# Kernel tuning notes

Hardware: AMD Instinct MI355X
Metric: run time of the kernel (lower is better)

The kernel has to match this reference:

```python
import jax, jax.numpy as jnp
import numpy as np
from jax import lax

N_SAMPLES1 = 128   # self.n_samples[0]
K = 64             # k in sample_and_group
RADIUS = 0.4       # self.radius[0]
BN_EPS = 1e-5
NEG_INF = -1e8
DIMS0 = [6, 64, 64, 128]      # mlps_in[0][0] -> mlps[0]
DIMS1 = [131, 128, 128, 512]  # 128+3 -> mlps[1] (use_light_weight=False)


def _fps(pos, n):
    # pos: (N,3) -> (n,) indices; deterministic start at point 0
    Np = pos.shape[0]
    def body(carry, _):
        dists, last = carry
        d = jnp.sum((pos - pos[last]) ** 2, axis=-1)
        dists = jnp.minimum(dists, d)
        return (dists, jnp.argmax(dists).astype(jnp.int32)), last
    _, idxs = lax.scan(body, (jnp.full((Np,), 1e10, pos.dtype), jnp.int32(0)), None, length=n)
    return idxs


def _gather(values, idx):
    # values (B,N,C), idx (B,...) -> (B,...,C)
    return jax.vmap(lambda v, i: v[i])(values, idx)


def _conv_bn_relu(x, W, b, g, be):
    # 1x1 Conv2d + BatchNorm2d (training-mode batch stats) + ReLU; x (B,n,k,Cin)
    y = jnp.einsum('bnkc,cd->bnkd', x, W) + b
    m = jnp.mean(y, axis=(0, 1, 2), keepdims=True)
    v = jnp.mean(jnp.square(y - m), axis=(0, 1, 2), keepdims=True)
    return jax.nn.relu((y - m) * lax.rsqrt(v + BN_EPS) * g + be)


def _forward(x, pos,
             W00, b00, g00, be00, W01, b01, g01, be01, W02, b02, g02, be02,
             W10, b10, g10, be10, W11, b11, g11, be11, W12, b12, g12, be12):
    # ---- stage 0: FPS + kNN grouping + conv-MLP + radius-masked max pool ----
    fidx = jax.vmap(lambda p: _fps(p, N_SAMPLES1))(pos)          # (B,128)
    sp = _gather(pos, fidx)                                      # (B,128,3) sampled_pos
    # squared pairwise distances (||a||^2+||b||^2-2ab); topk/mask on sq dist is
    # equivalent to topk/mask on sqrt dist (monotone), avoids sqrt(0) NaN grads
    sq = (jnp.sum(sp ** 2, -1)[:, :, None] + jnp.sum(pos ** 2, -1)[:, None, :]
          - 2.0 * jnp.einsum('bmd,bnd->bmn', sp, pos))           # (B,128,N)
    sq = jnp.maximum(sq, 0.0)
    neg, tidx = lax.top_k(-sq, K)                                # smallest-k
    topk_sq = -neg                                               # (B,128,64)
    gp = _gather(pos, tidx) - sp[:, :, None, :]                  # centered grouped pos
    gf = jnp.concatenate([gp, _gather(x, tidx)], axis=-1)        # (B,128,64,6)
    for (W, b, g, be) in ((W00, b00, g00, be00), (W01, b01, g01, be01), (W02, b02, g02, be02)):
        gf = _conv_bn_relu(gf, W, b, g, be)                      # (B,128,64,128)
    mask = topk_sq <= RADIUS * RADIUS
    x1 = jnp.max(jnp.where(mask[..., None], gf, NEG_INF), axis=2)  # (B,128,128)
    # ---- stage 1: global (n_samples == 1) ----
    g2 = jnp.concatenate([sp, x1], axis=-1)[:, None]             # (B,1,128,131)
    for (W, b, g, be) in ((W10, b10, g10, be10), (W11, b11, g11, be11), (W12, b12, g12, be12)):
        g2 = _conv_bn_relu(g2, W, b, g, be)                      # (B,1,128,512)
    global_x = jnp.max(g2[:, 0], axis=1, keepdims=True)          # (B,1,512)
    return global_x


def setup_inputs() -> dict:
    key = jax.random.key(0)
    ks = jax.random.split(key, 16)
    B, N = 16, 8192
    inp = {
        'x': jax.random.normal(ks[0], (B, N, 3), jnp.float32),
        'pos': jax.random.uniform(ks[1], (B, N, 3), jnp.float32),
    }
    ki = 2
    for li, dims in enumerate([DIMS0, DIMS1]):
        for ci in range(3):
            cin, cout = dims[ci], dims[ci + 1]
            inp[f'W{li}{ci}'] = jax.random.normal(ks[ki], (cin, cout), jnp.float32) * 0.05
            inp[f'b{li}{ci}'] = jnp.zeros((cout,), jnp.float32)
            inp[f'g{li}{ci}'] = jnp.ones((cout,), jnp.float32)
            inp[f'be{li}{ci}'] = jnp.zeros((cout,), jnp.float32)
            ki += 1
    return inp


def reference(x, pos,
              W00, b00, g00, be00, W01, b01, g01, be01, W02, b02, g02, be02,
              W10, b10, g10, be10, W11, b11, g11, be11, W12, b12, g12, be12):
    global_x = _forward(x, pos,
                        W00, b00, g00, be00, W01, b01, g01, be01, W02, b02, g02, be02,
                        W10, b10, g10, be10, W11, b11, g11, be11, W12, b12, g12, be12)
    pos_out = jnp.zeros((pos.shape[0], 1, 3), pos.dtype)
    return global_x, pos_out
```

## Files before the change

kernel.cpp:

```cpp
#include <hip/hip_runtime.h>
#include <cstdint>
#include <cstddef>

#define NPTS 8192
#define BATCH 16
#define MS 128
#define KNB 64
#define NBLK (BATCH * MS)

__device__ __forceinline__ float dpp_wave_max_f32(float v) {
  v = fmaxf(v, __int_as_float(__builtin_amdgcn_update_dpp((int)0xff800000, __float_as_int(v), 0x111, 0xf, 0xf, false)));
  v = fmaxf(v, __int_as_float(__builtin_amdgcn_update_dpp((int)0xff800000, __float_as_int(v), 0x112, 0xf, 0xf, false)));
  v = fmaxf(v, __int_as_float(__builtin_amdgcn_update_dpp((int)0xff800000, __float_as_int(v), 0x114, 0xf, 0xf, false)));
  v = fmaxf(v, __int_as_float(__builtin_amdgcn_update_dpp((int)0xff800000, __float_as_int(v), 0x118, 0xf, 0xf, false)));
  v = fmaxf(v, __int_as_float(__builtin_amdgcn_update_dpp((int)0xff800000, __float_as_int(v), 0x142, 0xa, 0xf, false)));
  v = fmaxf(v, __int_as_float(__builtin_amdgcn_update_dpp((int)0xff800000, __float_as_int(v), 0x143, 0xc, 0xf, false)));
  return v;
}

__device__ __forceinline__ float dpp_wave_min_f32(float v) {
  v = fminf(v, __int_as_float(__builtin_amdgcn_update_dpp(0x7f800000, __float_as_int(v), 0x111, 0xf, 0xf, false)));
  v = fminf(v, __int_as_float(__builtin_amdgcn_update_dpp(0x7f800000, __float_as_int(v), 0x112, 0xf, 0xf, false)));
  v = fminf(v, __int_as_float(__builtin_amdgcn_update_dpp(0x7f800000, __float_as_int(v), 0x114, 0xf, 0xf, false)));
  v = fminf(v, __int_as_float(__builtin_amdgcn_update_dpp(0x7f800000, __float_as_int(v), 0x118, 0xf, 0xf, false)));
  v = fminf(v, __int_as_float(__builtin_amdgcn_update_dpp(0x7f800000, __float_as_int(v), 0x142, 0xa, 0xf, false)));
  v = fminf(v, __int_as_float(__builtin_amdgcn_update_dpp(0x7f800000, __float_as_int(v), 0x143, 0xc, 0xf, false)));
  return v;
}

__device__ __forceinline__ unsigned dpp_wave_min_u32(unsigned v) {
  unsigned o;
  o = (unsigned)__builtin_amdgcn_update_dpp((int)0xffffffffu, (int)v, 0x111, 0xf, 0xf, false); v = (o < v) ? o : v;
  o = (unsigned)__builtin_amdgcn_update_dpp((int)0xffffffffu, (int)v, 0x112, 0xf, 0xf, false); v = (o < v) ? o : v;
  o = (unsigned)__builtin_amdgcn_update_dpp((int)0xffffffffu, (int)v, 0x114, 0xf, 0xf, false); v = (o < v) ? o : v;
  o = (unsigned)__builtin_amdgcn_update_dpp((int)0xffffffffu, (int)v, 0x118, 0xf, 0xf, false); v = (o < v) ? o : v;
  o = (unsigned)__builtin_amdgcn_update_dpp((int)0xffffffffu, (int)v, 0x142, 0xa, 0xf, false); v = (o < v) ? o : v;
  o = (unsigned)__builtin_amdgcn_update_dpp((int)0xffffffffu, (int)v, 0x143, 0xc, 0xf, false); v = (o < v) ? o : v;
  return v;
}

__device__ __forceinline__ float dpp_row_max_f32(float v) {
  v = fmaxf(v, __int_as_float(__builtin_amdgcn_update_dpp((int)0xff800000, __float_as_int(v), 0x111, 0xf, 0xf, false)));
  v = fmaxf(v, __int_as_float(__builtin_amdgcn_update_dpp((int)0xff800000, __float_as_int(v), 0x112, 0xf, 0xf, false)));
  v = fmaxf(v, __int_as_float(__builtin_amdgcn_update_dpp((int)0xff800000, __float_as_int(v), 0x114, 0xf, 0xf, false)));
  v = fmaxf(v, __int_as_float(__builtin_amdgcn_update_dpp((int)0xff800000, __float_as_int(v), 0x118, 0xf, 0xf, false)));
  return v;
}

__device__ __forceinline__ unsigned dpp_row_min_u32(unsigned v) {
  unsigned o;
  o = (unsigned)__builtin_amdgcn_update_dpp((int)0xffffffffu, (int)v, 0x111, 0xf, 0xf, false); v = (o < v) ? o : v;
  o = (unsigned)__builtin_amdgcn_update_dpp((int)0xffffffffu, (int)v, 0x112, 0xf, 0xf, false); v = (o < v) ? o : v;
  o = (unsigned)__builtin_amdgcn_update_dpp((int)0xffffffffu, (int)v, 0x114, 0xf, 0xf, false); v = (o < v) ? o : v;
  o = (unsigned)__builtin_amdgcn_update_dpp((int)0xffffffffu, (int)v, 0x118, 0xf, 0xf, false); v = (o < v) ? o : v;
  return v;
}

#define FPS_STEP(J)                                                        \
  {                                                                        \
    const float4 p = pts4[J * 1024 + t];                                   \
    const float dx = p.x - lx;                                             \
    const float dy = p.y - ly;                                             \
    const float dz = p.z - lz;                                             \
    const float d = dx * dx + dy * dy + dz * dz;                           \
    md##J = fminf(md##J, d);                                               \
  }

#define FPS_RESCAN(J)                                                      \
  if (md##J == wv) best = (unsigned)(J * 1024 + t);

__global__ __launch_bounds__(1024, 4) void fps_kernel(const float* __restrict__ pos,
                                                      float* __restrict__ sp,
                                                      float* __restrict__ mdst,
                                                      float* __restrict__ lastst,
                                                      int it0) {
#pragma clang fp contract(off)
  extern __shared__ float4 pts4[];
  __shared__ float wval[2][16];
  __shared__ unsigned widx[2][16];
  const int b = blockIdx.x;
  const float* P = pos + (size_t)b * NPTS * 3;
  const int t = threadIdx.x;
  const int wave = t >> 6;
  const int lane = t & 63;
  float md0, md1, md2, md3, md4, md5, md6, md7;
  for (int i = t; i < NPTS; i += 1024)
    pts4[i] = make_float4(P[i * 3 + 0], P[i * 3 + 1], P[i * 3 + 2], 0.f);
  float lx, ly, lz;
  float* M = mdst + ((size_t)b * 1024 + t) * 8;
  if (it0 == 0) {
    md0 = md1 = md2 = md3 = md4 = md5 = md6 = md7 = 1e10f;
    lx = P[0]; ly = P[1]; lz = P[2];
  } else {
    const float4 a = *reinterpret_cast<const float4*>(M);
    const float4 c = *reinterpret_cast<const float4*>(M + 4);
    md0 = a.x; md1 = a.y; md2 = a.z; md3 = a.w;
    md4 = c.x; md5 = c.y; md6 = c.z; md7 = c.w;
    lx = lastst[b * 4 + 0]; ly = lastst[b * 4 + 1]; lz = lastst[b * 4 + 2];
  }
  __syncthreads();
  for (int it = it0; it < it0 + MS / 2; ++it) {
    if (t == 0) {
      sp[((size_t)b * MS + it) * 3 + 0] = lx;
      sp[((size_t)b * MS + it) * 3 + 1] = ly;
      sp[((size_t)b * MS + it) * 3 + 2] = lz;
    }
    FPS_STEP(0) FPS_STEP(1) FPS_STEP(2) FPS_STEP(3)
    FPS_STEP(4) FPS_STEP(5) FPS_STEP(6) FPS_STEP(7)
    const float m01 = fmaxf(md0, md1), m23 = fmaxf(md2, md3);
    const float m45 = fmaxf(md4, md5), m67 = fmaxf(md6, md7);
    const float bv = fmaxf(fmaxf(m01, m23), fmaxf(m45, m67));
    const float wv = __int_as_float(
        __builtin_amdgcn_readlane(__float_as_int(dpp_wave_max_f32(bv)), 63));
    unsigned best = 0xffffffffu;
    if (bv == wv) {
      FPS_RESCAN(7) FPS_RESCAN(6) FPS_RESCAN(5) FPS_RESCAN(4)
      FPS_RESCAN(3) FPS_RESCAN(2) FPS_RESCAN(1) FPS_RESCAN(0)
    }
    const unsigned wi =
        (unsigned)__builtin_amdgcn_readlane((int)dpp_wave_min_u32(best), 63);
    const int par = it & 1;
    if (lane == 0) { wval[par][wave] = wv; widx[par][wave] = wi; }
    __syncthreads();
    const float a = wval[par][lane & 15];
    const float Mx = __int_as_float(
        __builtin_amdgcn_readlane(__float_as_int(dpp_row_max_f32(a)), 15));
    const unsigned c2 = (a == Mx) ? widx[par][lane & 15] : 0xffffffffu;
    const unsigned idx =
        (unsigned)__builtin_amdgcn_readlane((int)dpp_row_min_u32(c2), 15);
    const float4 c = pts4[idx];
    lx = c.x; ly = c.y; lz = c.z;
  }
  {
    float4 a, c;
    a.x = md0; a.y = md1; a.z = md2; a.w = md3;
    c.x = md4; c.y = md5; c.z = md6; c.w = md7;
    *reinterpret_cast<float4*>(M) = a;
    *reinterpret_cast<float4*>(M + 4) = c;
    if (t == 0) {
      lastst[b * 4 + 0] = lx;
      lastst[b * 4 + 1] = ly;
      lastst[b * 4 + 2] = lz;
    }
  }
}

__global__ __launch_bounds__(256) void knn_kernel(const float* __restrict__ pos,
                                                  const float* __restrict__ xf,
                                                  const float* __restrict__ sp,
                                                  float* __restrict__ gf0,
                                                  float* __restrict__ sqsel) {
#pragma clang fp contract(off)
  __shared__ float sqv[NPTS + 32];
  __shared__ unsigned long long wlist[4][KNB];
  __shared__ unsigned long long selk[KNB];
  const int bm = blockIdx.x;
  const int b = bm >> 7;
  const float* P = pos + (size_t)b * NPTS * 3;
  const float sx = sp[bm * 3 + 0], sy = sp[bm * 3 + 1], sz = sp[bm * 3 + 2];
  const float nsp = sx * sx + sy * sy + sz * sz;
  const int t = threadIdx.x;
  const int wave = t >> 6;
  const int lane = t & 63;
  float cv;
  unsigned ci;
  {
    unsigned long long k0 = ~0ULL;
    for (int j = 0; j < 32; ++j) {
      const int i = j * 256 + t;
      const float qx = P[i * 3 + 0], qy = P[i * 3 + 1], qz = P[i * 3 + 2];
      const float npos = qx * qx + qy * qy + qz * qz;
      const float dt = sx * qx + sy * qy + sz * qz;
      float sq = (nsp + npos) - 2.0f * dt;
      sq = fmaxf(sq, 0.0f);
      sqv[i + j] = sq;
      const unsigned long long key =
          ((unsigned long long)__float_as_uint(sq) << 32) | (unsigned)i;
      if (key < k0) k0 = key;
    }
    cv = __uint_as_float((unsigned)(k0 >> 32));
    ci = (unsigned)k0;
  }
  __syncthreads();
  unsigned cmask = 0u;
  for (int round = 0; round < KNB; ++round) {
    const float wv = __int_as_float(
        __builtin_amdgcn_readlane(__float_as_int(dpp_wave_min_f32(cv)), 63));
    const unsigned sel = (cv == wv) ? ci : 0xffffffffu;
    const unsigned wi =
        (unsigned)__builtin_amdgcn_readlane((int)dpp_wave_min_u32(sel), 63);
    if (lane == 0)
      wlist[wave][round] =
          ((unsigned long long)__float_as_uint(wv) << 32) | wi;
    const int col = (int)(wi & 255u);
    const int ownerLane = col & 63;
    const unsigned jsel = wi >> 8;
    if (lane == ownerLane) cmask |= (1u << jsel);
    const unsigned omask =
        (unsigned)__builtin_amdgcn_readlane((int)cmask, ownerLane);
    float v = __uint_as_float(0x7f800000u);
    unsigned ii = 0xffffffffu;
    if (lane < 32 && !((omask >> lane) & 1u)) {
      const int i = lane * 256 + col;
      v = sqv[i + lane];
      ii = (unsigned)i;
    }
    const float mv = __int_as_float(
        __builtin_amdgcn_readlane(__float_as_int(dpp_wave_min_f32(v)), 63));
    const unsigned s2 = (v == mv) ? ii : 0xffffffffu;
    const unsigned mi =
        (unsigned)__builtin_amdgcn_readlane((int)dpp_wave_min_u32(s2), 63);
    if (lane == ownerLane) { cv = mv; ci = mi; }
  }
  __syncthreads();
  {
    const int w = wave, r = lane;
    const unsigned long long e = wlist[w][r];
    int rank = r;
#pragma unroll
    for (int w2 = 0; w2 < 4; ++w2) {
      if (w2 == w) continue;
      int lo = 0;
#pragma unroll
      for (int step = 32; step > 0; step >>= 1)
        if (lo + step <= KNB && wlist[w2][lo + step - 1] < e) lo += step;
      rank += lo;
    }
    if (rank < KNB) selk[rank] = e;
  }
  __syncthreads();
  if (t < KNB) {
    const unsigned long long e = selk[t];
    const int i = (int)(e & 0xffffffffu);
    const float* X = xf + (size_t)b * NPTS * 3;
    const size_t base = ((size_t)bm * KNB + t) * 6;
    gf0[base + 0] = P[i * 3 + 0] - sx;
    gf0[base + 1] = P[i * 3 + 1] - sy;
    gf0[base + 2] = P[i * 3 + 2] - sz;
    gf0[base + 3] = X[i * 3 + 0];
    gf0[base + 4] = X[i * 3 + 1];
    gf0[base + 5] = X[i * 3 + 2];
    sqsel[(size_t)bm * KNB + t] = __uint_as_float((unsigned)(e >> 32));
  }
}

__global__ __launch_bounds__(256) void l1_kernel(
    const float* __restrict__ gf0, const float* __restrict__ W0,
    const float* __restrict__ B0,
    float* __restrict__ psum, float* __restrict__ psq,
    float* __restrict__ y1pre) {
  __shared__ float in6[64 * 8];
  __shared__ float wbuf[384];
  __shared__ float out[64 * 65];
  const int blk = blockIdx.x;
  const int t = threadIdx.x;
  const float* G = gf0 + (size_t)blk * 384;
  for (int i = t; i < 384; i += 256) in6[(i / 6) * 8 + (i % 6)] = G[i];
  for (int i = t; i < 384; i += 256) wbuf[i] = W0[i];
  __syncthreads();
  const int r = t >> 2;
  const int c0 = (t & 3) * 16;
  float acc[16];
#pragma unroll
  for (int j = 0; j < 16; ++j) acc[j] = B0[c0 + j];
  for (int cin = 0; cin < 6; ++cin) {
    const float a = in6[r * 8 + cin];
#pragma unroll
    for (int j = 0; j < 16; ++j) acc[j] = fmaf(a, wbuf[cin * 64 + c0 + j], acc[j]);
  }
#pragma unroll
  for (int j = 0; j < 16; ++j) out[r * 65 + c0 + j] = acc[j];
  __syncthreads();
  if (t < 64) {
    float s = 0.f, q = 0.f;
    for (int r2 = 0; r2 < 64; ++r2) { const float v = out[r2 * 65 + t]; s += v; q += v * v; }
    psum[(size_t)t * NBLK + blk] = s;
    psq[(size_t)t * NBLK + blk] = q;
  }
  float* Y = y1pre + (size_t)blk * 4096;
  for (int i = t; i < 4096; i += 256) Y[i] = out[(i >> 6) * 65 + (i & 63)];
}

__global__ __launch_bounds__(256) void l2_kernel(
    const float* __restrict__ ypre, const float* __restrict__ sc,
    const float* __restrict__ sh, const float* __restrict__ W1,
    const float* __restrict__ B1,
    float* __restrict__ psum, float* __restrict__ psq,
    float* __restrict__ yout) {
  __shared__ float As[64 * 68];
  __shared__ float Bs[64 * 64];
  __shared__ float out[64 * 68];
  const int blk = blockIdx.x;
  const int t = threadIdx.x;
  const float* Y = ypre + (size_t)blk * 4096;
  for (int i = t; i < 4096; i += 256) {
    const int c = i & 63;
    As[(i >> 6) * 68 + c] = fmaxf(fmaf(Y[i], sc[c], sh[c]), 0.f);
  }
  for (int i = t; i < 4096; i += 256) Bs[i] = W1[i];
  __syncthreads();
  const int tr = t >> 4;
  const int tc4 = (t & 15) * 4;
  float acc[4][4];
#pragma unroll
  for (int s = 0; s < 4; ++s)
#pragma unroll
    for (int j = 0; j < 4; ++j) acc[s][j] = B1[tc4 + j];
  for (int k0 = 0; k0 < 64; k0 += 4) {
    float4 av[4];
#pragma unroll
    for (int s = 0; s < 4; ++s)
      av[s] = *reinterpret_cast<const float4*>(&As[(tr + 16 * s) * 68 + k0]);
#pragma unroll
    for (int kk = 0; kk < 4; ++kk) {
      const float4 bv = *reinterpret_cast<const float4*>(&Bs[(k0 + kk) * 64 + tc4]);
#pragma unroll
      for (int s = 0; s < 4; ++s) {
        const float a = (kk == 0) ? av[s].x : (kk == 1) ? av[s].y
                       : (kk == 2) ? av[s].z : av[s].w;
        acc[s][0] = fmaf(a, bv.x, acc[s][0]);
        acc[s][1] = fmaf(a, bv.y, acc[s][1]);
        acc[s][2] = fmaf(a, bv.z, acc[s][2]);
        acc[s][3] = fmaf(a, bv.w, acc[s][3]);
      }
    }
  }
#pragma unroll
  for (int s = 0; s < 4; ++s) {
    float4 o;
    o.x = acc[s][0]; o.y = acc[s][1]; o.z = acc[s][2]; o.w = acc[s][3];
    *reinterpret_cast<float4*>(&out[(tr + 16 * s) * 68 + tc4]) = o;
  }
  __syncthreads();
  if (t < 64) {
    float s = 0.f, q = 0.f;
    for (int r2 = 0; r2 < 64; ++r2) { const float v = out[r2 * 68 + t]; s += v; q += v * v; }
    psum[(size_t)t * NBLK + blk] = s;
    psq[(size_t)t * NBLK + blk] = q;
  }
  float* O = yout + (size_t)blk * 4096;
  for (int i = t; i < 4096; i += 256) O[i] = out[(i >> 6) * 68 + (i & 63)];
}

__global__ __launch_bounds__(256) void l3_kernel(
    const float* __restrict__ ypre, const float* __restrict__ sc,
    const float* __restrict__ sh, const float* __restrict__ W2,
    const float* __restrict__ B2,
    float* __restrict__ psum, float* __restrict__ psq,
    float* __restrict__ yout) {
  __shared__ float As[64 * 68];
  __shared__ float Bs[64 * 64];
  __shared__ float out[64 * 68];
  const int blk = blockIdx.x;
  const int t = threadIdx.x;
  const float* Y = ypre + (size_t)blk * 4096;
  for (int i = t; i < 4096; i += 256) {
    const int c = i & 63;
    As[(i >> 6) * 68 + c] = fmaxf(fmaf(Y[i], sc[c], sh[c]), 0.f);
  }
  const int tr = t >> 4;
  const int tc4 = (t & 15) * 4;
  for (int hc = 0; hc < 2; ++hc) {
    __syncthreads();
    for (int i = t; i < 4096; i += 256)
      Bs[i] = W2[(i >> 6) * 128 + hc * 64 + (i & 63)];
    __syncthreads();
    float acc[4][4];
#pragma unroll
    for (int s = 0; s < 4; ++s)
#pragma unroll
      for (int j = 0; j < 4; ++j) acc[s][j] = B2[hc * 64 + tc4 + j];
    for (int k0 = 0; k0 < 64; k0 += 4) {
      float4 av[4];
#pragma unroll
      for (int s = 0; s < 4; ++s)
        av[s] = *reinterpret_cast<const float4*>(&As[(tr + 16 * s) * 68 + k0]);
#pragma unroll
      for (int kk = 0; kk < 4; ++kk) {
        const float4 bv = *reinterpret_cast<const float4*>(&Bs[(k0 + kk) * 64 + tc4]);
#pragma unroll
        for (int s = 0; s < 4; ++s) {
          const float a = (kk == 0) ? av[s].x : (kk == 1) ? av[s].y
                         : (kk == 2) ? av[s].z : av[s].w;
          acc[s][0] = fmaf(a, bv.x, acc[s][0]);
          acc[s][1] = fmaf(a, bv.y, acc[s][1]);
          acc[s][2] = fmaf(a, bv.z, acc[s][2]);
          acc[s][3] = fmaf(a, bv.w, acc[s][3]);
        }
      }
    }
#pragma unroll
    for (int s = 0; s < 4; ++s) {
      float4 o;
      o.x = acc[s][0]; o.y = acc[s][1]; o.z = acc[s][2]; o.w = acc[s][3];
      *reinterpret_cast<float4*>(&out[(tr + 16 * s) * 68 + tc4]) = o;
    }
    __syncthreads();
    if (t < 64) {
      float s = 0.f, q = 0.f;
      for (int r2 = 0; r2 < 64; ++r2) { const float v = out[r2 * 68 + t]; s += v; q += v * v; }
      psum[(size_t)(hc * 64 + t) * NBLK + blk] = s;
      psq[(size_t)(hc * 64 + t) * NBLK + blk] = q;
    }
    float* O = yout + (size_t)blk * 8192;
    for (int i = t; i < 4096; i += 256)
      O[(i >> 6) * 128 + hc * 64 + (i & 63)] = out[(i >> 6) * 68 + (i & 63)];
  }
}

__global__ __launch_bounds__(128) void l4s1_kernel(
    const float* __restrict__ y3pre, const float* __restrict__ sc3,
    const float* __restrict__ sh3, const float* __restrict__ sqsel,
    const float* __restrict__ sp, const float* __restrict__ W,
    const float* __restrict__ bia, float* __restrict__ y1) {
  __shared__ float sqs[64];
  __shared__ float row[132];
  const int blk = blockIdx.x;
  const int t = threadIdx.x;
  if (t < 64) sqs[t] = sqsel[(size_t)blk * 64 + t];
  __syncthreads();
  const float scv = sc3[t], shv = sh3[t];
  const float* Y = y3pre + (size_t)blk * 8192;
  float mx = -1e8f;
  for (int r = 0; r < 64; ++r) {
    const float act = fmaxf(fmaf(Y[r * 128 + t], scv, shv), 0.f);
    const float v = (sqs[r] <= 0.16f) ? act : -1e8f;
    mx = fmaxf(mx, v);
  }
  if (t < 3) row[t] = sp[(size_t)blk * 3 + t];
  row[3 + t] = mx;
  __syncthreads();
  float acc = bia[t];
  for (int cin = 0; cin < 131; ++cin) acc = fmaf(row[cin], W[(size_t)cin * 128 + t], acc);
  y1[(size_t)blk * 128 + t] = acc;
}

__global__ __launch_bounds__(256) void p_stats(const float* __restrict__ psum,
                                               const float* __restrict__ psq,
                                               float invN,
                                               const float* __restrict__ g,
                                               const float* __restrict__ be,
                                               float* __restrict__ sc,
                                               float* __restrict__ sh) {
  const int c = blockIdx.x;
  const int t = threadIdx.x;
  double s = 0.0, q = 0.0;
  for (int k = t; k < NBLK; k += 256) {
    s += (double)psum[(size_t)c * NBLK + k];
    q += (double)psq[(size_t)c * NBLK + k];
  }
  __shared__ double ss[256], qq[256];
  ss[t] = s;
  qq[t] = q;
  __syncthreads();
  for (int st = 128; st > 0; st >>= 1) {
    if (t < st) { ss[t] += ss[t + st]; qq[t] += qq[t + st]; }
    __syncthreads();
  }
  if (t == 0) {
    const double mean = ss[0] * (double)invN;
    double var = qq[0] * (double)invN - mean * mean;
    if (var < 0.0) var = 0.0;
    const float scl = (float)((double)g[c] / sqrt(var + 1e-5));
    sc[c] = scl;
    sh[c] = be[c] - (float)mean * scl;
  }
}

__global__ __launch_bounds__(128) void s2_kernel(const float* __restrict__ y1,
                                                 const float* __restrict__ sc, const float* __restrict__ sh,
                                                 const float* __restrict__ W, const float* __restrict__ bia,
                                                 float* __restrict__ y2) {
  __shared__ float row[128];
  const int rowid = blockIdx.x;
  const int t = threadIdx.x;
  row[t] = fmaxf(fmaf(y1[(size_t)rowid * 128 + t], sc[t], sh[t]), 0.f);
  __syncthreads();
  float acc = bia[t];
  for (int cin = 0; cin < 128; ++cin) acc = fmaf(row[cin], W[(size_t)cin * 128 + t], acc);
  y2[(size_t)rowid * 128 + t] = acc;
}

__global__ __launch_bounds__(256) void s3_kernel(const float* __restrict__ y2,
                                                 const float* __restrict__ sc, const float* __restrict__ sh,
                                                 const float* __restrict__ W, const float* __restrict__ bia,
                                                 float* __restrict__ y3) {
  __shared__ float row[128];
  const int rowid = blockIdx.x;
  const int t = threadIdx.x;
  if (t < 128) row[t] = fmaxf(fmaf(y2[(size_t)rowid * 128 + t], sc[t], sh[t]), 0.f);
  __syncthreads();
  for (int h = 0; h < 2; ++h) {
    const int c = h * 256 + t;
    float acc = bia[c];
    for (int cin = 0; cin < 128; ++cin) acc = fmaf(row[cin], W[(size_t)cin * 512 + c], acc);
    y3[(size_t)rowid * 512 + c] = acc;
  }
}

__global__ __launch_bounds__(256) void s_stats(const float* __restrict__ y, int C, int rows,
                                               const float* __restrict__ g, const float* __restrict__ be,
                                               float* __restrict__ sc, float* __restrict__ sh) {
  const int c = blockIdx.x;
  const int t = threadIdx.x;
  double s = 0.0, q = 0.0;
  for (int r2 = t; r2 < rows; r2 += 256) {
    const double v = (double)y[(size_t)r2 * C + c];
    s += v;
    q += v * v;
  }
  __shared__ double ss[256], qq[256];
  ss[t] = s;
  qq[t] = q;
  __syncthreads();
  for (int st = 128; st > 0; st >>= 1) {
    if (t < st) { ss[t] += ss[t + st]; qq[t] += qq[t + st]; }
    __syncthreads();
  }
  if (t == 0) {
    const double mean = ss[0] / rows;
    double var = qq[0] / rows - mean * mean;
    if (var < 0.0) var = 0.0;
    const float scl = (float)((double)g[c] / sqrt(var + 1e-5));
    sc[c] = scl;
    sh[c] = be[c] - (float)mean * scl;
  }
}

__global__ __launch_bounds__(256) void s_stats_final(const float* __restrict__ y3,
                                                     const float* __restrict__ g,
                                                     const float* __restrict__ be,
                                                     float* __restrict__ out) {
  const int c = blockIdx.x;
  const int t = threadIdx.x;
  double s = 0.0, q = 0.0;
  for (int r2 = t; r2 < NBLK; r2 += 256) {
    const double v = (double)y3[(size_t)r2 * 512 + c];
    s += v;
    q += v * v;
  }
  __shared__ double ss[256], qq[256];
  __shared__ float sscl, sshv;
  ss[t] = s;
  qq[t] = q;
  __syncthreads();
  for (int st = 128; st > 0; st >>= 1) {
    if (t < st) { ss[t] += ss[t + st]; qq[t] += qq[t + st]; }
    __syncthreads();
  }
  if (t == 0) {
    const double mean = ss[0] / NBLK;
    double var = qq[0] / NBLK - mean * mean;
    if (var < 0.0) var = 0.0;
    const float scl = (float)((double)g[c] / sqrt(var + 1e-5));
    sscl = scl;
    sshv = be[c] - (float)mean * scl;
  }
  __syncthreads();
  const float scl = sscl, shv = sshv;
  float mx = -3.402823466e+38f;
  for (int k = 0; k < 8; ++k) {
    const int r = t * 8 + k;
    const float v = fmaxf(fmaf(y3[(size_t)r * 512 + c], scl, shv), 0.f);
    mx = fmaxf(mx, v);
  }
  __shared__ float pmax[256];
  pmax[t] = mx;
  __syncthreads();
  if (t < 16) {
    float m = -3.402823466e+38f;
    for (int j = 0; j < 16; ++j) m = fmaxf(m, pmax[t * 16 + j]);
    out[(size_t)t * 512 + c] = m;
  }
  if (c == 0 && t < 48) out[8192 + t] = 0.f;
}

extern "C" void kernel_launch(void* const* d_in, const int* in_sizes, int n_in,
                              void* d_out, int out_size, void* d_ws, size_t ws_size,
                              hipStream_t stream) {
  const float* x    = (const float*)d_in[0];
  const float* pos  = (const float*)d_in[1];
  const float* W00  = (const float*)d_in[2];
  const float* b00  = (const float*)d_in[3];
  const float* g00  = (const float*)d_in[4];
  const float* be00 = (const float*)d_in[5];
  const float* W01  = (const float*)d_in[6];
  const float* b01  = (const float*)d_in[7];
  const float* g01  = (const float*)d_in[8];
  const float* be01 = (const float*)d_in[9];
  const float* W02  = (const float*)d_in[10];
  const float* b02  = (const float*)d_in[11];
  const float* g02  = (const float*)d_in[12];
  const float* be02 = (const float*)d_in[13];
  const float* W10  = (const float*)d_in[14];
  const float* b10  = (const float*)d_in[15];
  const float* g10  = (const float*)d_in[16];
  const float* be10 = (const float*)d_in[17];
  const float* W11  = (const float*)d_in[18];
  const float* b11  = (const float*)d_in[19];
  const float* g11  = (const float*)d_in[20];
  const float* be11 = (const float*)d_in[21];
  const float* W12  = (const float*)d_in[22];
  const float* b12  = (const float*)d_in[23];
  const float* g12  = (const float*)d_in[24];
  const float* be12 = (const float*)d_in[25];

  float* w = (float*)d_ws;
  float* sp    = w;
  float* gf0   = sp + 6144;
  float* sqsel = gf0 + 786432;
  float* x1    = sqsel + 131072;
  float* parts = x1 + 262144;
  float* psum  = parts;
  float* psq   = parts + 128 * NBLK;
  float* st    = parts + 524288;
  float* sc1 = st + 0,    *sh1 = st + 64;
  float* sc2 = st + 128,  *sh2 = st + 192;
  float* sc3 = st + 256,  *sh3 = st + 384;
  float* t1sc = st + 512, *t1sh = st + 640;
  float* t2sc = st + 768, *t2sh = st + 896;
  float* y1s = st + 2048;
  float* y2s = y1s + 262144;
  float* y3s = y2s + 262144;
  const size_t BASE = 3284992;
  float* y1pre = w + BASE;
  float* y2pre = y1pre + 8388608;
  float* y3pre = y2pre + 8388608;
  float* mdws  = y3pre + 16777216;
  float* lastw = mdws + 131072;

  fps_kernel<<<BATCH, 1024, NPTS * sizeof(float4), stream>>>(pos, sp, mdws, lastw, 0);
  fps_kernel<<<BATCH, 1024, NPTS * sizeof(float4), stream>>>(pos, sp, mdws, lastw, 64);
  knn_kernel<<<BATCH * MS, 256, 0, stream>>>(pos, x, sp, gf0, sqsel);

  const float invN0 = 1.0f / (float)(NBLK * KNB);
  l1_kernel<<<NBLK, 256, 0, stream>>>(gf0, W00, b00, psum, psq, y1pre);
  p_stats<<<64, 256, 0, stream>>>(psum, psq, invN0, g00, be00, sc1, sh1);
  l2_kernel<<<NBLK, 256, 0, stream>>>(y1pre, sc1, sh1, W01, b01, psum, psq, y2pre);
  p_stats<<<64, 256, 0, stream>>>(psum, psq, invN0, g01, be01, sc2, sh2);
  l3_kernel<<<NBLK, 256, 0, stream>>>(y2pre, sc2, sh2, W02, b02, psum, psq, y3pre);
  p_stats<<<128, 256, 0, stream>>>(psum, psq, invN0, g02, be02, sc3, sh3);
  l4s1_kernel<<<NBLK, 128, 0, stream>>>(y3pre, sc3, sh3, sqsel, sp, W10, b10, y1s);

  s_stats<<<128, 256, 0, stream>>>(y1s, 128, NBLK, g10, be10, t1sc, t1sh);
  s2_kernel<<<NBLK, 128, 0, stream>>>(y1s, t1sc, t1sh, W11, b11, y2s);
  s_stats<<<128, 256, 0, stream>>>(y2s, 128, NBLK, g11, be11, t2sc, t2sh);
  s3_kernel<<<NBLK, 256, 0, stream>>>(y2s, t2sc, t2sh, W12, b12, y3s);
  s_stats_final<<<512, 256, 0, stream>>>(y3s, g12, be12, (float*)d_out);
}
```

Baseline: 433.8 us.

## Fuse FPS and kNN into one cooperative kernel with progress-flag overlap

Replaces the two-launch FPS and the separate kNN kernel with one cooperative kernel. Sixteen blocks run farthest-point sampling for all 128 iterations and publish per-batch progress counters. The remaining 240 blocks each handle four kNN queries at once (one per 256-thread group) and spin on those counters, so grouping starts while sampling is still running. This hides the serial FPS latency behind kNN work and saves launches and the mdst/last-point state round trip. The cost is spin-waiting, reliance on every block being co-resident, and kNN blocks competing with FPS blocks for compute units.

```diff
diff --git a/kernel.cpp b/kernel.cpp
--- a/kernel.cpp
+++ b/kernel.cpp
@@ -7,6 +7,12 @@
 #define MS 128
 #define KNB 64
 #define NBLK (BATCH * MS)
+#define KNNBLK 240
+#define NQUAD 512
+#define SQV_Q 8224
+#define WL_OFF (4 * SQV_Q * 4)
+#define SELK_OFF (WL_OFF + 8192)
+#define DYN_BYTES (SELK_OFF + 2048)
 
 __device__ __forceinline__ float dpp_wave_max_f32(float v) {
   v = fmaxf(v, __int_as_float(__builtin_amdgcn_update_dpp((int)0xff800000, __float_as_int(v), 0x111, 0xf, 0xf, false)));
@@ -69,178 +75,174 @@
 #define FPS_RESCAN(J)                                                      \
   if (md##J == wv) best = (unsigned)(J * 1024 + t);
 
-__global__ __launch_bounds__(1024, 4) void fps_kernel(const float* __restrict__ pos,
-                                                      float* __restrict__ sp,
-                                                      float* __restrict__ mdst,
-                                                      float* __restrict__ lastst,
-                                                      int it0) {
+__global__ __launch_bounds__(1024, 4) void fk_kernel(const float* __restrict__ pos,
+                                                     const float* __restrict__ xf,
+                                                     float* __restrict__ sp,
+                                                     float* __restrict__ gf0,
+                                                     float* __restrict__ sqsel,
+                                                     int* __restrict__ prog) {
 #pragma clang fp contract(off)
-  extern __shared__ float4 pts4[];
-  __shared__ float wval[2][16];
-  __shared__ unsigned widx[2][16];
-  const int b = blockIdx.x;
-  const float* P = pos + (size_t)b * NPTS * 3;
-  const int t = threadIdx.x;
-  const int wave = t >> 6;
-  const int lane = t & 63;
-  float md0, md1, md2, md3, md4, md5, md6, md7;
-  for (int i = t; i < NPTS; i += 1024)
-    pts4[i] = make_float4(P[i * 3 + 0], P[i * 3 + 1], P[i * 3 + 2], 0.f);
-  float lx, ly, lz;
-  float* M = mdst + ((size_t)b * 1024 + t) * 8;
-  if (it0 == 0) {
-    md0 = md1 = md2 = md3 = md4 = md5 = md6 = md7 = 1e10f;
-    lx = P[0]; ly = P[1]; lz = P[2];
+  extern __shared__ char dynls[];
+  const int blk = blockIdx.x;
+  const int tid = threadIdx.x;
+  if (blk < BATCH) {
+    float4* pts4 = reinterpret_cast<float4*>(dynls);
+    __shared__ float wval[2][16];
+    __shared__ unsigned widx[2][16];
+    const int b = blk;
+    const float* P = pos + (size_t)b * NPTS * 3;
+    const int t = tid;
+    const int wave = t >> 6;
+    const int lane = t & 63;
+    float md0 = 1e10f, md1 = 1e10f, md2 = 1e10f, md3 = 1e10f;
+    float md4 = 1e10f, md5 = 1e10f, md6 = 1e10f, md7 = 1e10f;
+    for (int i = t; i < NPTS; i += 1024)
+      pts4[i] = make_float4(P[i * 3 + 0], P[i * 3 + 1], P[i * 3 + 2], 0.f);
+    float lx = P[0], ly = P[1], lz = P[2];
+    __syncthreads();
+    for (int it = 0; it < MS; ++it) {
+      if (t == 0) {
+        sp[((size_t)b * MS + it) * 3 + 0] = lx;
+        sp[((size_t)b * MS + it) * 3 + 1] = ly;
+        sp[((size_t)b * MS + it) * 3 + 2] = lz;
+        __hip_atomic_store(&prog[b], it + 1, __ATOMIC_RELEASE,
+                           __HIP_MEMORY_SCOPE_AGENT);
+      }
+      FPS_STEP(0) FPS_STEP(1) FPS_STEP(2) FPS_STEP(3)
+      FPS_STEP(4) FPS_STEP(5) FPS_STEP(6) FPS_STEP(7)
+      const float m01 = fmaxf(md0, md1), m23 = fmaxf(md2, md3);
+      const float m45 = fmaxf(md4, md5), m67 = fmaxf(md6, md7);
+      const float bv = fmaxf(fmaxf(m01, m23), fmaxf(m45, m67));
+      const float wv = __int_as_float(
+          __builtin_amdgcn_readlane(__float_as_int(dpp_wave_max_f32(bv)), 63));
+      unsigned best = 0xffffffffu;
+      if (bv == wv) {
+        FPS_RESCAN(7) FPS_RESCAN(6) FPS_RESCAN(5) FPS_RESCAN(4)
+        FPS_RESCAN(3) FPS_RESCAN(2) FPS_RESCAN(1) FPS_RESCAN(0)
+      }
+      const unsigned wi =
+          (unsigned)__builtin_amdgcn_readlane((int)dpp_wave_min_u32(best), 63);
+      const int par = it & 1;
+      if (lane == 0) { wval[par][wave] = wv; widx[par][wave] = wi; }
+      __syncthreads();
+      const float a = wval[par][lane & 15];
+      const float Mx = __int_as_float(
+          __builtin_amdgcn_readlane(__float_as_int(dpp_row_max_f32(a)), 15));
+      const unsigned c2 = (a == Mx) ? widx[par][lane & 15] : 0xffffffffu;
+      const unsigned idx =
+          (unsigned)__builtin_amdgcn_readlane((int)dpp_row_min_u32(c2), 15);
+      const float4 c = pts4[idx];
+      lx = c.x; ly = c.y; lz = c.z;
+    }
   } else {
-    const float4 a = *reinterpret_cast<const float4*>(M);
-    const float4 c = *reinterpret_cast<const float4*>(M + 4);
-    md0 = a.x; md1 = a.y; md2 = a.z; md3 = a.w;
-    md4 = c.x; md5 = c.y; md6 = c.z; md7 = c.w;
-    lx = lastst[b * 4 + 0]; ly = lastst[b * 4 + 1]; lz = lastst[b * 4 + 2];
-  }
-  __syncthreads();
-  for (int it = it0; it < it0 + MS / 2; ++it) {
-    if (t == 0) {
-      sp[((size_t)b * MS + it) * 3 + 0] = lx;
-      sp[((size_t)b * MS + it) * 3 + 1] = ly;
-      sp[((size_t)b * MS + it) * 3 + 2] = lz;
+    const int k = blk - BATCH;
+    const int q = tid >> 8;
+    const int t = tid & 255;
+    const int wave = t >> 6;
+    const int lane = tid & 63;
+    float* sqv = reinterpret_cast<float*>(dynls) + q * SQV_Q;
+    unsigned long long* wl =
+        reinterpret_cast<unsigned long long*>(dynls + WL_OFF) + (size_t)q * 256;
+    unsigned long long* selk =
+        reinterpret_cast<unsigned long long*>(dynls + SELK_OFF) + (size_t)q * 64;
+    for (int Q = k; Q < NQUAD; Q += KNNBLK) {
+      const int m = Q >> 2;
+      const int g = Q & 3;
+      const int batch = 4 * g + q;
+      if (tid == 0) {
+        for (int bb = 0; bb < 4; ++bb)
+          while (__hip_atomic_load(&prog[4 * g + bb], __ATOMIC_ACQUIRE,
+                                   __HIP_MEMORY_SCOPE_AGENT) <= m) {}
+      }
+      __syncthreads();
+      (void)__hip_atomic_load(&prog[batch], __ATOMIC_ACQUIRE,
+                              __HIP_MEMORY_SCOPE_AGENT);
+      const int bm = batch * MS + m;
+      const float* P = pos + (size_t)batch * NPTS * 3;
+      const float sx = sp[bm * 3 + 0], sy = sp[bm * 3 + 1], sz = sp[bm * 3 + 2];
+      const float nsp = sx * sx + sy * sy + sz * sz;
+      float cv;
+      unsigned ci;
+      {
+        unsigned long long k0 = ~0ULL;
+        for (int j = 0; j < 32; ++j) {
+          const int i = j * 256 + t;
+          const float qx = P[i * 3 + 0], qy = P[i * 3 + 1], qz = P[i * 3 + 2];
+          const float npos = qx * qx + qy * qy + qz * qz;
+          const float dt = sx * qx + sy * qy + sz * qz;
+          float sq = (nsp + npos) - 2.0f * dt;
+          sq = fmaxf(sq, 0.0f);
+          sqv[i + j] = sq;
+          const unsigned long long key =
+              ((unsigned long long)__float_as_uint(sq) << 32) | (unsigned)i;
+          if (key < k0) k0 = key;
+        }
+        cv = __uint_as_float((unsigned)(k0 >> 32));
+        ci = (unsigned)k0;
+      }
+      __syncthreads();
+      unsigned cmask = 0u;
+      for (int round = 0; round < KNB; ++round) {
+        const float wv = __int_as_float(
+            __builtin_amdgcn_readlane(__float_as_int(dpp_wave_min_f32(cv)), 63));
+        const unsigned sel = (cv == wv) ? ci : 0xffffffffu;
+        const unsigned wi =
+            (unsigned)__builtin_amdgcn_readlane((int)dpp_wave_min_u32(sel), 63);
+        if (lane == 0)
+          wl[wave * 64 + round] =
+              ((unsigned long long)__float_as_uint(wv) << 32) | wi;
+        const int col = (int)(wi & 255u);
+        const int ownerLane = col & 63;
+        const unsigned jsel = wi >> 8;
+        if (lane == ownerLane) cmask |= (1u << jsel);
+        const unsigned omask =
+            (unsigned)__builtin_amdgcn_readlane((int)cmask, ownerLane);
+        float v = __uint_as_float(0x7f800000u);
+        unsigned ii = 0xffffffffu;
+        if (lane < 32 && !((omask >> lane) & 1u)) {
+          const int i = lane * 256 + col;
+          v = sqv[i + lane];
+          ii = (unsigned)i;
+        }
+        const float mv = __int_as_float(
+            __builtin_amdgcn_readlane(__float_as_int(dpp_wave_min_f32(v)), 63));
+        const unsigned s2 = (v == mv) ? ii : 0xffffffffu;
+        const unsigned mi =
+            (unsigned)__builtin_amdgcn_readlane((int)dpp_wave_min_u32(s2), 63);
+        if (lane == ownerLane) { cv = mv; ci = mi; }
+      }
+      __syncthreads();
+      {
+        const int w = wave, r = lane;
+        const unsigned long long e = wl[w * 64 + r];
+        int rank = r;
+#pragma unroll
+        for (int w2 = 0; w2 < 4; ++w2) {
+          if (w2 == w) continue;
+          int lo = 0;
+#pragma unroll
+          for (int step = 32; step > 0; step >>= 1)
+            if (lo + step <= KNB && wl[w2 * 64 + lo + step - 1] < e) lo += step;
+          rank += lo;
+        }
+        if (rank < KNB) selk[rank] = e;
+      }
+      __syncthreads();
+      if (t < KNB) {
+        const unsigned long long e = selk[t];
+        const int i = (int)(e & 0xffffffffu);
+        const float* X = xf + (size_t)batch * NPTS * 3;
+        const size_t base = ((size_t)bm * KNB + t) * 6;
+        gf0[base + 0] = P[i * 3 + 0] - sx;
+        gf0[base + 1] = P[i * 3 + 1] - sy;
+        gf0[base + 2] = P[i * 3 + 2] - sz;
+        gf0[base + 3] = X[i * 3 + 0];
+        gf0[base + 4] = X[i * 3 + 1];
+        gf0[base + 5] = X[i * 3 + 2];
+        sqsel[(size_t)bm * KNB + t] = __uint_as_float((unsigned)(e >> 32));
+      }
+      __syncthreads();
     }
-    FPS_STEP(0) FPS_STEP(1) FPS_STEP(2) FPS_STEP(3)
-    FPS_STEP(4) FPS_STEP(5) FPS_STEP(6) FPS_STEP(7)
-    const float m01 = fmaxf(md0, md1), m23 = fmaxf(md2, md3);
-    const float m45 = fmaxf(md4, md5), m67 = fmaxf(md6, md7);
-    const float bv = fmaxf(fmaxf(m01, m23), fmaxf(m45, m67));
-    const float wv = __int_as_float(
-        __builtin_amdgcn_readlane(__float_as_int(dpp_wave_max_f32(bv)), 63));
-    unsigned best = 0xffffffffu;
-    if (bv == wv) {
-      FPS_RESCAN(7) FPS_RESCAN(6) FPS_RESCAN(5) FPS_RESCAN(4)
-      FPS_RESCAN(3) FPS_RESCAN(2) FPS_RESCAN(1) FPS_RESCAN(0)
-    }
-    const unsigned wi =
-        (unsigned)__builtin_amdgcn_readlane((int)dpp_wave_min_u32(best), 63);
-    const int par = it & 1;
-    if (lane == 0) { wval[par][wave] = wv; widx[par][wave] = wi; }
-    __syncthreads();
-    const float a = wval[par][lane & 15];
-    const float Mx = __int_as_float(
-        __builtin_amdgcn_readlane(__float_as_int(dpp_row_max_f32(a)), 15));
-    const unsigned c2 = (a == Mx) ? widx[par][lane & 15] : 0xffffffffu;
-    const unsigned idx =
-        (unsigned)__builtin_amdgcn_readlane((int)dpp_row_min_u32(c2), 15);
-    const float4 c = pts4[idx];
-    lx = c.x; ly = c.y; lz = c.z;
-  }
-  {
-    float4 a, c;
-    a.x = md0; a.y = md1; a.z = md2; a.w = md3;
-    c.x = md4; c.y = md5; c.z = md6; c.w = md7;
-    *reinterpret_cast<float4*>(M) = a;
-    *reinterpret_cast<float4*>(M + 4) = c;
-    if (t == 0) {
-      lastst[b * 4 + 0] = lx;
-      lastst[b * 4 + 1] = ly;
-      lastst[b * 4 + 2] = lz;
-    }
-  }
-}
-
-__global__ __launch_bounds__(256) void knn_kernel(const float* __restrict__ pos,
-                                                  const float* __restrict__ xf,
-                                                  const float* __restrict__ sp,
-                                                  float* __restrict__ gf0,
-                                                  float* __restrict__ sqsel) {
-#pragma clang fp contract(off)
-  __shared__ float sqv[NPTS + 32];
-  __shared__ unsigned long long wlist[4][KNB];
-  __shared__ unsigned long long selk[KNB];
-  const int bm = blockIdx.x;
-  const int b = bm >> 7;
-  const float* P = pos + (size_t)b * NPTS * 3;
-  const float sx = sp[bm * 3 + 0], sy = sp[bm * 3 + 1], sz = sp[bm * 3 + 2];
-  const float nsp = sx * sx + sy * sy + sz * sz;
-  const int t = threadIdx.x;
-  const int wave = t >> 6;
-  const int lane = t & 63;
-  float cv;
-  unsigned ci;
-  {
-    unsigned long long k0 = ~0ULL;
-    for (int j = 0; j < 32; ++j) {
-      const int i = j * 256 + t;
-      const float qx = P[i * 3 + 0], qy = P[i * 3 + 1], qz = P[i * 3 + 2];
-      const float npos = qx * qx + qy * qy + qz * qz;
-      const float dt = sx * qx + sy * qy + sz * qz;
-      float sq = (nsp + npos) - 2.0f * dt;
-      sq = fmaxf(sq, 0.0f);
-      sqv[i + j] = sq;
-      const unsigned long long key =
-          ((unsigned long long)__float_as_uint(sq) << 32) | (unsigned)i;
-      if (key < k0) k0 = key;
-    }
-    cv = __uint_as_float((unsigned)(k0 >> 32));
-    ci = (unsigned)k0;
-  }
-  __syncthreads();
-  unsigned cmask = 0u;
-  for (int round = 0; round < KNB; ++round) {
-    const float wv = __int_as_float(
-        __builtin_amdgcn_readlane(__float_as_int(dpp_wave_min_f32(cv)), 63));
-    const unsigned sel = (cv == wv) ? ci : 0xffffffffu;
-    const unsigned wi =
-        (unsigned)__builtin_amdgcn_readlane((int)dpp_wave_min_u32(sel), 63);
-    if (lane == 0)
-      wlist[wave][round] =
-          ((unsigned long long)__float_as_uint(wv) << 32) | wi;
-    const int col = (int)(wi & 255u);
-    const int ownerLane = col & 63;
-    const unsigned jsel = wi >> 8;
-    if (lane == ownerLane) cmask |= (1u << jsel);
-    const unsigned omask =
-        (unsigned)__builtin_amdgcn_readlane((int)cmask, ownerLane);
-    float v = __uint_as_float(0x7f800000u);
-    unsigned ii = 0xffffffffu;
-    if (lane < 32 && !((omask >> lane) & 1u)) {
-      const int i = lane * 256 + col;
-      v = sqv[i + lane];
-      ii = (unsigned)i;
-    }
-    const float mv = __int_as_float(
-        __builtin_amdgcn_readlane(__float_as_int(dpp_wave_min_f32(v)), 63));
-    const unsigned s2 = (v == mv) ? ii : 0xffffffffu;
-    const unsigned mi =
-        (unsigned)__builtin_amdgcn_readlane((int)dpp_wave_min_u32(s2), 63);
-    if (lane == ownerLane) { cv = mv; ci = mi; }
-  }
-  __syncthreads();
-  {
-    const int w = wave, r = lane;
-    const unsigned long long e = wlist[w][r];
-    int rank = r;
-#pragma unroll
-    for (int w2 = 0; w2 < 4; ++w2) {
-      if (w2 == w) continue;
-      int lo = 0;
-#pragma unroll
-      for (int step = 32; step > 0; step >>= 1)
-        if (lo + step <= KNB && wlist[w2][lo + step - 1] < e) lo += step;
-      rank += lo;
-    }
-    if (rank < KNB) selk[rank] = e;
-  }
-  __syncthreads();
-  if (t < KNB) {
-    const unsigned long long e = selk[t];
-    const int i = (int)(e & 0xffffffffu);
-    const float* X = xf + (size_t)b * NPTS * 3;
-    const size_t base = ((size_t)bm * KNB + t) * 6;
-    gf0[base + 0] = P[i * 3 + 0] - sx;
-    gf0[base + 1] = P[i * 3 + 1] - sy;
-    gf0[base + 2] = P[i * 3 + 2] - sz;
-    gf0[base + 3] = X[i * 3 + 0];
-    gf0[base + 4] = X[i * 3 + 1];
-    gf0[base + 5] = X[i * 3 + 2];
-    sqsel[(size_t)bm * KNB + t] = __uint_as_float((unsigned)(e >> 32));
   }
 }
 
@@ -626,12 +628,21 @@
   float* y1pre = w + BASE;
   float* y2pre = y1pre + 8388608;
   float* y3pre = y2pre + 8388608;
-  float* mdws  = y3pre + 16777216;
-  float* lastw = mdws + 131072;
-
-  fps_kernel<<<BATCH, 1024, NPTS * sizeof(float4), stream>>>(pos, sp, mdws, lastw, 0);
-  fps_kernel<<<BATCH, 1024, NPTS * sizeof(float4), stream>>>(pos, sp, mdws, lastw, 64);
-  knn_kernel<<<BATCH * MS, 256, 0, stream>>>(pos, x, sp, gf0, sqsel);
+  int*   prog  = (int*)(y3pre + 16777216);
+
+  hipMemsetAsync(prog, 0, BATCH * sizeof(int), stream);
+  {
+    const float* a0 = pos;
+    const float* a1 = x;
+    float* a2 = sp;
+    float* a3 = gf0;
+    float* a4 = sqsel;
+    int* a5 = prog;
+    void* args[6] = {(void*)&a0, (void*)&a1, (void*)&a2,
+                     (void*)&a3, (void*)&a4, (void*)&a5};
+    hipLaunchCooperativeKernel((const void*)fk_kernel, dim3(256), dim3(1024),
+                               args, DYN_BYTES, stream);
+  }
 
   const float invN0 = 1.0f / (float)(NBLK * KNB);
   l1_kernel<<<NBLK, 256, 0, stream>>>(gf0, W00, b00, psum, psq, y1pre);
```

Measured after the change: 612.1 us. 1.41x slower.
